# Optimization experiments

Hardware: AMD Instinct MI355X
Metric: run time of the kernel (lower is better)

The kernel has to match this reference:

```python
import jax, jax.numpy as jnp
import numpy as np

N_NODES = 50000
N_EDGES = 640000
N_GRAPHS = 64
IN_DIM, HID, OUT_DIM = 128, 256, 4


def gcn_conv(x, src, dst, W, b, n_nodes):
    """PyG GCNConv: linear transform, then sym-normalized aggregation with self-loops."""
    h = x @ W  # [N, out]
    deg = jnp.zeros((n_nodes,), h.dtype).at[dst].add(1.0) + 1.0  # +1 self-loop
    dinv = jax.lax.rsqrt(deg)  # deg >= 1 always
    norm = dinv[src] * dinv[dst]  # [E]
    msg = h[src] * norm[:, None]  # [E, out]  gather + scale
    agg = jax.ops.segment_sum(msg, dst, num_segments=n_nodes)  # scatter-add
    agg = agg + h * (dinv * dinv)[:, None]  # self-loop contribution
    return agg + b


def global_mean_pool(x, batch, num_graphs):
    s = jax.ops.segment_sum(x, batch, num_segments=num_graphs)
    cnt = jax.ops.segment_sum(jnp.ones((x.shape[0],), x.dtype), batch, num_segments=num_graphs)
    return s / jnp.clip(cnt, 1.0)[:, None]


def setup_inputs() -> dict:
    key = jax.random.key(0)
    ks = jax.random.split(key, 8)
    x = jax.random.normal(ks[0], (N_NODES, IN_DIM), jnp.float32)
    src = jax.random.randint(ks[1], (N_EDGES,), 0, N_NODES, jnp.int64 if jax.config.jax_enable_x64 else jnp.int32)
    dst = jax.random.randint(ks[2], (N_EDGES,), 0, N_NODES, src.dtype)
    batch = jnp.sort(jax.random.randint(ks[3], (N_NODES,), 0, N_GRAPHS, src.dtype))
    W1 = jax.random.normal(ks[4], (IN_DIM, HID), jnp.float32) * (1.0 / np.sqrt(IN_DIM))
    b1 = jnp.zeros((HID,), jnp.float32)
    W2 = jax.random.normal(ks[5], (HID, HID // 2), jnp.float32) * (1.0 / np.sqrt(HID))
    b2 = jnp.zeros((HID // 2,), jnp.float32)
    Wfc = jax.random.normal(ks[6], (HID // 2, OUT_DIM), jnp.float32) * (1.0 / np.sqrt(HID // 2))
    bfc = jnp.zeros((OUT_DIM,), jnp.float32)
    return {"x": x, "src": src, "dst": dst, "batch": batch,
            "W1": W1, "b1": b1, "W2": W2, "b2": b2, "Wfc": Wfc, "bfc": bfc}


def reference(x, src, dst, batch, W1, b1, W2, b2, Wfc, bfc):
    n = x.shape[0]
    h = jax.nn.relu(gcn_conv(x, src, dst, W1, b1, n))   # dropout is identity at inference
    h = jax.nn.relu(gcn_conv(h, src, dst, W2, b2, n))
    g = global_mean_pool(h, batch, N_GRAPHS)            # [G, HID//2]
    return g @ Wfc + bfc                                # [G, OUT_DIM]
```

## Files before the change

### kernel.cpp

```cpp
#include <hip/hip_runtime.h>


constexpr int IN_DIM  = 128;
constexpr int HID     = 256;
constexpr int HID2    = 128;
constexpr int OUT_DIM = 4;
constexpr int NGRAPH  = 64;
constexpr int TP      = 132;

typedef __attribute__((ext_vector_type(8))) short bf16x8;
typedef __attribute__((ext_vector_type(4))) float f32x4;

__device__ __forceinline__ short f2bf(float f) {
    union { float f; unsigned u; } v; v.f = f;
    unsigned r = v.u + 0x7fff + ((v.u >> 16) & 1);
    return (short)(r >> 16);
}
__device__ __forceinline__ float bf2f(short s) {
    union { unsigned u; float f; } v; v.u = ((unsigned)(unsigned short)s) << 16;
    return v.f;
}


__global__ void wprep_all_kernel(const float* __restrict__ W1, short* __restrict__ W1th,
                                 short* __restrict__ W1tl,
                                 const float* __restrict__ W2, short* __restrict__ W2th,
                                 short* __restrict__ W2tl,
                                 int* __restrict__ count, float* __restrict__ pool, int N) {
    int i = blockIdx.x * blockDim.x + threadIdx.x;
    if (i < IN_DIM * HID) {
        int k = i / HID, n = i % HID;
        float w = W1[i];
        short h = f2bf(w);
        W1th[n * IN_DIM + k] = h;
        W1tl[n * IN_DIM + k] = f2bf(w - bf2f(h));
    }
    if (i < HID * HID2) {
        int k = i / HID2, n = i % HID2;
        float w = W2[i];
        short h = f2bf(w);
        W2th[n * HID + k] = h;
        W2tl[n * HID + k] = f2bf(w - bf2f(h));
    }
    if (i < N) count[i] = 0;
    if (i < NGRAPH * HID2) pool[i] = 0.f;
}


__global__ void hist_kernel(const int* __restrict__ dst, int* __restrict__ count,
                            ushort* __restrict__ rank, int E) {
    int i = blockIdx.x * blockDim.x + threadIdx.x;
    if (i < E) rank[i] = (ushort)atomicAdd(&count[dst[i]], 1);
}

__global__ void scan1_kernel(const int* __restrict__ count, int* __restrict__ bsums, int N) {
    __shared__ int s[256];
    int t = threadIdx.x, i = blockIdx.x * 256 + t;
    int v = (i < N) ? count[i] : 0;
    s[t] = v; __syncthreads();
    for (int o = 1; o < 256; o <<= 1) {
        int x = (t >= o) ? s[t - o] : 0;
        __syncthreads(); s[t] += x; __syncthreads();
    }
    if (t == 255) bsums[blockIdx.x] = s[255];
}

__global__ void scan3_kernel(const int* __restrict__ count, const int* __restrict__ bsums,
                             int* __restrict__ rowptr, float* __restrict__ dinv,
                             int N, int E, int nb) {
    __shared__ int sb[256];
    __shared__ int s[256];
    int t = threadIdx.x, i = blockIdx.x * 256 + t;
    int bv = (t < nb) ? bsums[t] : 0;
    sb[t] = bv; __syncthreads();
    for (int o = 1; o < 256; o <<= 1) {
        int x = (t >= o) ? sb[t - o] : 0;
        __syncthreads(); sb[t] += x; __syncthreads();
    }
    int myex = (blockIdx.x == 0) ? 0 : sb[blockIdx.x - 1];
    int v = (i < N) ? count[i] : 0;
    s[t] = v; __syncthreads();
    for (int o = 1; o < 256; o <<= 1) {
        int x = (t >= o) ? s[t - o] : 0;
        __syncthreads(); s[t] += x; __syncthreads();
    }
    if (i < N) {
        rowptr[i] = myex + s[t] - v;
        dinv[i] = rsqrtf((float)v + 1.0f);
        if (i == 0) rowptr[N] = E;
    }
}

__global__ void scatter_scale_kernel(const int* __restrict__ src, const int* __restrict__ dst,
                                     const ushort* __restrict__ rank,
                                     const int* __restrict__ rowptr, ushort* __restrict__ csr,
                                     const float* __restrict__ x, const float* __restrict__ dinv,
                                     ushort* __restrict__ xb, int E, int total2) {
    int i = blockIdx.x * blockDim.x + threadIdx.x;
    if (i < E) {
        int p = rowptr[dst[i]] + (int)rank[i];
        csr[p] = (ushort)src[i];
    }
    if (i < total2) {
        float d = dinv[i >> 6];
        float2 v = ((const float2*)x)[i];
        ushort2 o;
        o.x = (ushort)f2bf(v.x * d);
        o.y = (ushort)f2bf(v.y * d);
        ((ushort2*)xb)[i] = o;
    }
}


template <int K, int N, bool ALO, bool RELU, bool SCALED>
__launch_bounds__(256)
__global__ void gemm_tile_kernel(const short* __restrict__ Ah, const short* __restrict__ Al,
                                 const short* __restrict__ Bh, const short* __restrict__ Bl,
                                 const float* __restrict__ bias,
                                 const float* __restrict__ dinv,
                                 short* __restrict__ Cb, int M) {
    __shared__ __align__(16) short LDSBUF[128 * TP];
    short (*S)[8][512] = (short (*)[8][512])LDSBUF;

    const int tid  = threadIdx.x;
    const int wave = tid >> 6;
    const int lane = tid & 63;
    const int row0 = blockIdx.y * 128;
    const int col0 = blockIdx.x * 128;

    const int l15 = lane & 15;
    const int kq  = (lane >> 4) * 8;

    f32x4 acc[4][4];
#pragma unroll
    for (int i = 0; i < 4; ++i)
#pragma unroll
        for (int j = 0; j < 4; ++j) acc[i][j] = f32x4{0.f, 0.f, 0.f, 0.f};

    const int mt0 = (wave & 1) * 4;
    const int nt0 = (wave >> 1) * 4;

    for (int kb = 0; kb < K; kb += 32) {
        if (ALO) {
            const short* gsrc = (wave == 0) ? Ah : (wave == 1) ? Al : (wave == 2) ? Bh : Bl;
            const bool isA = wave < 2;
            const int rb = (isA ? row0 : col0) + l15;
            bf16x8 stg[8];
#pragma unroll
            for (int j = 0; j < 8; ++j) {
                int rr = rb + j * 16;
                if (isA && rr >= M) rr = M - 1;
                stg[j] = *(const bf16x8*)(gsrc + (size_t)rr * K + kb + kq);
            }
#pragma unroll
            for (int j = 0; j < 8; ++j)
                *(bf16x8*)&S[wave][j][lane * 8] = stg[j];
        } else {
            if (wave < 2) {
                const int rb = row0 + l15;
                bf16x8 stg[4];
#pragma unroll
                for (int j = 0; j < 4; ++j) {
                    int rr = rb + (wave * 4 + j) * 16;
                    if (rr >= M) rr = M - 1;
                    stg[j] = *(const bf16x8*)(Ah + (size_t)rr * K + kb + kq);
                }
#pragma unroll
                for (int j = 0; j < 4; ++j)
                    *(bf16x8*)&S[0][wave * 4 + j][lane * 8] = stg[j];
            } else {
                const short* gsrc = (wave == 2) ? Bh : Bl;
                const int rb = col0 + l15;
                bf16x8 stg[8];
#pragma unroll
                for (int j = 0; j < 8; ++j)
                    stg[j] = *(const bf16x8*)(gsrc + (size_t)(rb + j * 16) * K + kb + kq);
#pragma unroll
                for (int j = 0; j < 8; ++j)
                    *(bf16x8*)&S[wave][j][lane * 8] = stg[j];
            }
        }
        __syncthreads();

        bf16x8 ah[4], al[4], bh[4], bl[4];
#pragma unroll
        for (int i = 0; i < 4; ++i) {
            ah[i] = *(const bf16x8*)&S[0][mt0 + i][lane * 8];
            if (ALO) al[i] = *(const bf16x8*)&S[1][mt0 + i][lane * 8];
            bh[i] = *(const bf16x8*)&S[2][nt0 + i][lane * 8];
            bl[i] = *(const bf16x8*)&S[3][nt0 + i][lane * 8];
        }
#pragma unroll
        for (int i = 0; i < 4; ++i)
#pragma unroll
            for (int j = 0; j < 4; ++j) {
                acc[i][j] = __builtin_amdgcn_mfma_f32_16x16x32_bf16(ah[i], bh[j], acc[i][j], 0, 0, 0);
                acc[i][j] = __builtin_amdgcn_mfma_f32_16x16x32_bf16(ah[i], bl[j], acc[i][j], 0, 0, 0);
                if (ALO)
                    acc[i][j] = __builtin_amdgcn_mfma_f32_16x16x32_bf16(al[i], bh[j], acc[i][j], 0, 0, 0);
            }
        __syncthreads();
    }

    short* T = LDSBUF;
    const int lrow_b = (wave & 1) * 64 + (lane >> 4) * 4;
    const int lcol_b = (wave >> 1) * 64 + l15;
#pragma unroll
    for (int j = 0; j < 4; ++j) {
        int lcol = lcol_b + j * 16;
        float bv = RELU ? bias[col0 + lcol] : 0.f;
#pragma unroll
        for (int i = 0; i < 4; ++i) {
#pragma unroll
            for (int r = 0; r < 4; ++r) {
                int lrow = lrow_b + i * 16 + r;
                float v = acc[i][j][r];
                if (RELU) v = fmaxf(v + bv, 0.f);
                if (SCALED) {
                    int dr = row0 + lrow; if (dr >= M) dr = M - 1;
                    v *= dinv[dr];
                }
                T[lrow * TP + lcol] = f2bf(v);
            }
        }
    }
    __syncthreads();
#pragma unroll
    for (int it = 0; it < 8; ++it) {
        int chunk = it * 256 + tid;
        int lr = chunk >> 4;
        int lc = (chunk & 15) * 8;
        int grow = row0 + lr;
        if (grow < M)
            *(bf16x8*)(Cb + (size_t)grow * N + col0 + lc) = *(const bf16x8*)&T[lr * TP + lc];
    }
}


template <bool POOL>
__launch_bounds__(256)
__global__ void agg_group_kernel(const ushort* __restrict__ hb, const float* __restrict__ dinv,
                                 const int* __restrict__ rowptr, const ushort* __restrict__ csr,
                                 const float* __restrict__ bias,
                                 short* __restrict__ oh,
                                 const int* __restrict__ batch, float* __restrict__ pool,
                                 int N) {
    __shared__ float pacc[16][128];
    __shared__ int   sgid[16];

    const int tid  = threadIdx.x;
    const int li   = tid & 15;
    const int nib  = tid >> 4;
    const int node = blockIdx.x * 16 + nib;
    const bool valid = node < N;
    const int cw = valid ? node : N - 1;

    const int lo = rowptr[cw], hi = rowptr[cw + 1];
    const float dd = dinv[cw];

    float a[8];
    {
        bf16x8 sv = *(const bf16x8*)(hb + ((size_t)cw << 7) + (li << 3));
#pragma unroll
        for (int d = 0; d < 8; ++d) a[d] = bf2f(sv[d]);
    }

    const ushort* hsl = hb + (li << 3);

    for (int base = lo; base < hi; base += 16) {
        int cnt = min(16, hi - base);
        int sidx = (int)csr[base + (li < cnt ? li : cnt - 1)];
        bf16x8 p[8], q[8];
#pragma unroll
        for (int u = 0; u < 8; ++u) {
            int s = __shfl(sidx, u < cnt ? u : cnt - 1, 16);
            p[u] = *(const bf16x8*)(hsl + ((size_t)s << 7));
        }
#pragma unroll
        for (int u = 0; u < 8; ++u) {
            int e = 8 + u;
            int s = __shfl(sidx, e < cnt ? e : cnt - 1, 16);
            q[u] = *(const bf16x8*)(hsl + ((size_t)s << 7));
        }
#pragma unroll
        for (int u = 0; u < 8; ++u) {
            bool v = u < cnt;
#pragma unroll
            for (int d = 0; d < 8; ++d) a[d] += v ? bf2f(p[u][d]) : 0.f;
        }
#pragma unroll
        for (int u = 0; u < 8; ++u) {
            bool v = 8 + u < cnt;
#pragma unroll
            for (int d = 0; d < 8; ++d) a[d] += v ? bf2f(q[u][d]) : 0.f;
        }
    }

#pragma unroll
    for (int d = 0; d < 8; ++d) a[d] *= dd;

    if (!POOL) {
        if (valid) {
            bf16x8 o;
#pragma unroll
            for (int d = 0; d < 8; ++d) o[d] = f2bf(a[d]);
            *(bf16x8*)&oh[(size_t)node * 128 + li * 8] = o;
        }
        return;
    }

    {
        float4 b0 = ((const float4*)bias)[li * 2];
        float4 b1 = ((const float4*)bias)[li * 2 + 1];
        a[0] = fmaxf(a[0] + b0.x, 0.f); a[1] = fmaxf(a[1] + b0.y, 0.f);
        a[2] = fmaxf(a[2] + b0.z, 0.f); a[3] = fmaxf(a[3] + b0.w, 0.f);
        a[4] = fmaxf(a[4] + b1.x, 0.f); a[5] = fmaxf(a[5] + b1.y, 0.f);
        a[6] = fmaxf(a[6] + b1.z, 0.f); a[7] = fmaxf(a[7] + b1.w, 0.f);
    }
    if (li == 0) sgid[nib] = valid ? batch[node] : -1;
#pragma unroll
    for (int d = 0; d < 8; ++d) pacc[nib][li * 8 + d] = a[d];
    __syncthreads();
    if (tid < 128) {
        int c = tid;
        int cur = sgid[0];
        float run = 0.f;
#pragma unroll 1
        for (int w = 0; w < 16; ++w) {
            int gi = sgid[w];
            if (gi < 0) break;
            if (gi != cur) { atomicAdd(&pool[cur * HID2 + c], run); run = 0.f; cur = gi; }
            run += pacc[w][c];
        }
        atomicAdd(&pool[cur * HID2 + c], run);
    }
}


__device__ __forceinline__ int lower_bound_i(const int* __restrict__ a, int n, int key) {
    int lo = 0, hi = n;
    while (lo < hi) {
        int mid = (lo + hi) >> 1;
        if (a[mid] < key) lo = mid + 1; else hi = mid;
    }
    return lo;
}

__global__ void fc_kernel(const float* __restrict__ pool, const int* __restrict__ batch,
                          const float* __restrict__ Wfc, const float* __restrict__ bfc,
                          float* __restrict__ out, int N) {
    int t = threadIdx.x;
    int g = t >> 2, o = t & 3;
    int lo = lower_bound_i(batch, N, g);
    int hi = lower_bound_i(batch, N, g + 1);
    float acc = 0.f;
#pragma unroll 8
    for (int c = 0; c < HID2; ++c)
        acc = fmaf(pool[g * HID2 + c], Wfc[c * OUT_DIM + o], acc);
    float inv = 1.0f / fmaxf((float)(hi - lo), 1.0f);
    out[g * OUT_DIM + o] = acc * inv + bfc[o];
}

extern "C" void kernel_launch(void* const* d_in, const int* in_sizes, int n_in,
                              void* d_out, int out_size, void* d_ws, size_t ws_size,
                              hipStream_t stream) {
    const float* x   = (const float*)d_in[0];
    const int* src   = (const int*)d_in[1];
    const int* dst   = (const int*)d_in[2];
    const int* batch = (const int*)d_in[3];
    const float* W1  = (const float*)d_in[4];
    const float* b1  = (const float*)d_in[5];
    const float* W2  = (const float*)d_in[6];
    const float* b2  = (const float*)d_in[7];
    const float* Wfc = (const float*)d_in[8];
    const float* bfc = (const float*)d_in[9];
    float* out = (float*)d_out;

    const int N = in_sizes[0] / IN_DIM;
    const int E = in_sizes[1];
    const int NB = (N + 255) / 256;
    const int GA = (N + 15) / 16;

    char* ws = (char*)d_ws;
    size_t off = 0;
    auto alloc = [&](size_t bytes) {
        char* p = ws + off;
        off = (off + bytes + 255) & ~(size_t)255;
        return p;
    };
    float*  dinv   = (float*) alloc((size_t)N * 4);
    int*    count  = (int*)   alloc((size_t)N * 4);
    int*    rowptr = (int*)   alloc((size_t)(N + 1) * 4);
    int*    bsums  = (int*)   alloc(256 * 4);
    ushort* rank   = (ushort*)alloc((size_t)E * 2);
    ushort* csr    = (ushort*)alloc((size_t)E * 2);
    short*  W1th   = (short*) alloc((size_t)IN_DIM * HID * 2);
    short*  W1tl   = (short*) alloc((size_t)IN_DIM * HID * 2);
    short*  W2th   = (short*) alloc((size_t)HID * HID2 * 2);
    short*  W2tl   = (short*) alloc((size_t)HID * HID2 * 2);
    ushort* xb     = (ushort*)alloc((size_t)N * IN_DIM * 2);
    short*  axb    = (short*) alloc((size_t)N * IN_DIM * 2);
    short*  a1h    = (short*) alloc((size_t)N * HID * 2);
    float*  pool   = (float*) alloc((size_t)NGRAPH * HID2 * 4);
    ushort* h2b = xb;

    wprep_all_kernel<<<(max(IN_DIM * HID, N) + 255) / 256, 256, 0, stream>>>(
        W1, W1th, W1tl, W2, W2th, W2tl, count, pool, N);

    hist_kernel<<<(E + 255) / 256, 256, 0, stream>>>(dst, count, rank, E);
    scan1_kernel<<<NB, 256, 0, stream>>>(count, bsums, N);
    scan3_kernel<<<NB, 256, 0, stream>>>(count, bsums, rowptr, dinv, N, E, NB);
    scatter_scale_kernel<<<(N * 64 + 255) / 256, 256, 0, stream>>>(
        src, dst, rank, rowptr, csr, x, dinv, xb, E, N * 64);

    agg_group_kernel<false><<<GA, 256, 0, stream>>>(
        xb, dinv, rowptr, csr, nullptr, axb, nullptr, nullptr, N);
    gemm_tile_kernel<IN_DIM, HID, false, true, false>
        <<<dim3(HID / 128, (N + 127) / 128), 256, 0, stream>>>(
        axb, nullptr, W1th, W1tl, b1, nullptr, a1h, N);

    gemm_tile_kernel<HID, HID2, false, false, true>
        <<<dim3(HID2 / 128, (N + 127) / 128), 256, 0, stream>>>(
        a1h, nullptr, W2th, W2tl, nullptr, dinv, (short*)h2b, N);
    agg_group_kernel<true><<<GA, 256, 0, stream>>>(
        h2b, dinv, rowptr, csr, b2, nullptr, batch, pool, N);

    fc_kernel<<<1, NGRAPH * OUT_DIM, 0, stream>>>(pool, batch, Wfc, bfc, out, N);
}
```

Baseline: 242.7 us.

## Fuse both dense GEMMs into one kernel keeping hidden activations in LDS

Replaces the two tiled GEMM launches with one fused kernel. Each block takes 64 rows, computes relu(A·W1+b1) into LDS, then multiplies by W2 and scales by dinv before writing bf16 output. This removes the N×256 bf16 intermediate round trip through global memory and one launch. In exchange, weight fragments are now read directly from global/L2 without LDS sharing, and there are fewer blocks (64-row tiles). The non-pooling aggregation kernel also returns early for out-of-range threads.

```diff
diff --git a/kernel.cpp b/kernel.cpp
--- a/kernel.cpp
+++ b/kernel.cpp
@@ -6,7 +6,6 @@
 constexpr int HID2    = 128;
 constexpr int OUT_DIM = 4;
 constexpr int NGRAPH  = 64;
-constexpr int TP      = 132;
 
 typedef __attribute__((ext_vector_type(8))) short bf16x8;
 typedef __attribute__((ext_vector_type(4))) float f32x4;
@@ -112,127 +111,130 @@
 }
 
 
-template <int K, int N, bool ALO, bool RELU, bool SCALED>
 __launch_bounds__(256)
-__global__ void gemm_tile_kernel(const short* __restrict__ Ah, const short* __restrict__ Al,
-                                 const short* __restrict__ Bh, const short* __restrict__ Bl,
-                                 const float* __restrict__ bias,
+__global__ void mlp_fused_kernel(const short* __restrict__ A,
+                                 const short* __restrict__ W1h, const short* __restrict__ W1l,
+                                 const float* __restrict__ b1,
+                                 const short* __restrict__ W2h, const short* __restrict__ W2l,
                                  const float* __restrict__ dinv,
                                  short* __restrict__ Cb, int M) {
-    __shared__ __align__(16) short LDSBUF[128 * TP];
-    short (*S)[8][512] = (short (*)[8][512])LDSBUF;
+    __shared__ __align__(16) short L[16384 + 8448];
+    short* A1 = L;
+    short* A0 = L + 16384;
+    __shared__ float dinv_s[64];
 
     const int tid  = threadIdx.x;
-    const int wave = tid >> 6;
+    const int w    = tid >> 6;
     const int lane = tid & 63;
-    const int row0 = blockIdx.y * 128;
-    const int col0 = blockIdx.x * 128;
-
-    const int l15 = lane & 15;
-    const int kq  = (lane >> 4) * 8;
-
-    f32x4 acc[4][4];
-#pragma unroll
-    for (int i = 0; i < 4; ++i)
-#pragma unroll
-        for (int j = 0; j < 4; ++j) acc[i][j] = f32x4{0.f, 0.f, 0.f, 0.f};
-
-    const int mt0 = (wave & 1) * 4;
-    const int nt0 = (wave >> 1) * 4;
-
-    for (int kb = 0; kb < K; kb += 32) {
-        if (ALO) {
-            const short* gsrc = (wave == 0) ? Ah : (wave == 1) ? Al : (wave == 2) ? Bh : Bl;
-            const bool isA = wave < 2;
-            const int rb = (isA ? row0 : col0) + l15;
-            bf16x8 stg[8];
-#pragma unroll
-            for (int j = 0; j < 8; ++j) {
-                int rr = rb + j * 16;
-                if (isA && rr >= M) rr = M - 1;
-                stg[j] = *(const bf16x8*)(gsrc + (size_t)rr * K + kb + kq);
+    const int l15  = lane & 15;
+    const int kq8  = (lane >> 4) * 8;
+    const int row0 = blockIdx.x * 64;
+
+    {
+        int rr = row0 + w * 16 + l15; if (rr >= M) rr = M - 1;
+        const short* ap = A + (size_t)rr * IN_DIM + kq8;
+        bf16x8 stg[4];
+#pragma unroll
+        for (int ks = 0; ks < 4; ++ks) stg[ks] = *(const bf16x8*)(ap + ks * 32);
+#pragma unroll
+        for (int ks = 0; ks < 4; ++ks) *(bf16x8*)&A0[(w * 4 + ks) * 512 + lane * 8] = stg[ks];
+    }
+    if (tid < 64) { int r = row0 + tid; dinv_s[tid] = dinv[r < M ? r : M - 1]; }
+    __syncthreads();
+
+    f32x4 acc1[4][4];
+#pragma unroll
+    for (int m = 0; m < 4; ++m)
+#pragma unroll
+        for (int n = 0; n < 4; ++n) acc1[m][n] = f32x4{0.f, 0.f, 0.f, 0.f};
+
+    const short* w1hp = W1h + (size_t)(w * 64 + l15) * IN_DIM + kq8;
+    const short* w1lp = W1l + (size_t)(w * 64 + l15) * IN_DIM + kq8;
+#pragma unroll
+    for (int ks = 0; ks < 4; ++ks) {
+        bf16x8 af[4], bh[4], bl[4];
+#pragma unroll
+        for (int m = 0; m < 4; ++m) af[m] = *(const bf16x8*)&A0[(m * 4 + ks) * 512 + lane * 8];
+#pragma unroll
+        for (int n = 0; n < 4; ++n) {
+            bh[n] = *(const bf16x8*)(w1hp + (size_t)(n * 16) * IN_DIM + ks * 32);
+            bl[n] = *(const bf16x8*)(w1lp + (size_t)(n * 16) * IN_DIM + ks * 32);
+        }
+#pragma unroll
+        for (int m = 0; m < 4; ++m)
+#pragma unroll
+            for (int n = 0; n < 4; ++n) {
+                acc1[m][n] = __builtin_amdgcn_mfma_f32_16x16x32_bf16(af[m], bh[n], acc1[m][n], 0, 0, 0);
+                acc1[m][n] = __builtin_amdgcn_mfma_f32_16x16x32_bf16(af[m], bl[n], acc1[m][n], 0, 0, 0);
             }
-#pragma unroll
-            for (int j = 0; j < 8; ++j)
-                *(bf16x8*)&S[wave][j][lane * 8] = stg[j];
-        } else {
-            if (wave < 2) {
-                const int rb = row0 + l15;
-                bf16x8 stg[4];
-#pragma unroll
-                for (int j = 0; j < 4; ++j) {
-                    int rr = rb + (wave * 4 + j) * 16;
-                    if (rr >= M) rr = M - 1;
-                    stg[j] = *(const bf16x8*)(Ah + (size_t)rr * K + kb + kq);
-                }
-#pragma unroll
-                for (int j = 0; j < 4; ++j)
-                    *(bf16x8*)&S[0][wave * 4 + j][lane * 8] = stg[j];
-            } else {
-                const short* gsrc = (wave == 2) ? Bh : Bl;
-                const int rb = col0 + l15;
-                bf16x8 stg[8];
-#pragma unroll
-                for (int j = 0; j < 8; ++j)
-                    stg[j] = *(const bf16x8*)(gsrc + (size_t)(rb + j * 16) * K + kb + kq);
-#pragma unroll
-                for (int j = 0; j < 8; ++j)
-                    *(bf16x8*)&S[wave][j][lane * 8] = stg[j];
+    }
+
+#pragma unroll
+    for (int n = 0; n < 4; ++n) {
+        int c  = w * 64 + n * 16 + l15;
+        float bv = b1[c];
+        int ks = c >> 5;
+        int q  = (c >> 3) & 3;
+        int e  = c & 7;
+#pragma unroll
+        for (int m = 0; m < 4; ++m)
+#pragma unroll
+            for (int r4 = 0; r4 < 4; ++r4) {
+                int rl = (lane >> 4) * 4 + r4;
+                float v = fmaxf(acc1[m][n][r4] + bv, 0.f);
+                A1[(m * 8 + ks) * 512 + (rl + 16 * q) * 8 + e] = f2bf(v);
             }
-        }
-        __syncthreads();
-
-        bf16x8 ah[4], al[4], bh[4], bl[4];
-#pragma unroll
-        for (int i = 0; i < 4; ++i) {
-            ah[i] = *(const bf16x8*)&S[0][mt0 + i][lane * 8];
-            if (ALO) al[i] = *(const bf16x8*)&S[1][mt0 + i][lane * 8];
-            bh[i] = *(const bf16x8*)&S[2][nt0 + i][lane * 8];
-            bl[i] = *(const bf16x8*)&S[3][nt0 + i][lane * 8];
-        }
-#pragma unroll
-        for (int i = 0; i < 4; ++i)
-#pragma unroll
-            for (int j = 0; j < 4; ++j) {
-                acc[i][j] = __builtin_amdgcn_mfma_f32_16x16x32_bf16(ah[i], bh[j], acc[i][j], 0, 0, 0);
-                acc[i][j] = __builtin_amdgcn_mfma_f32_16x16x32_bf16(ah[i], bl[j], acc[i][j], 0, 0, 0);
-                if (ALO)
-                    acc[i][j] = __builtin_amdgcn_mfma_f32_16x16x32_bf16(al[i], bh[j], acc[i][j], 0, 0, 0);
+    }
+    __syncthreads();
+
+    f32x4 acc2[4][2];
+#pragma unroll
+    for (int m = 0; m < 4; ++m)
+#pragma unroll
+        for (int n = 0; n < 2; ++n) acc2[m][n] = f32x4{0.f, 0.f, 0.f, 0.f};
+
+    const short* w2hp = W2h + (size_t)(w * 32 + l15) * HID + kq8;
+    const short* w2lp = W2l + (size_t)(w * 32 + l15) * HID + kq8;
+#pragma unroll
+    for (int ks = 0; ks < 8; ++ks) {
+        bf16x8 af[4], bh[2], bl[2];
+#pragma unroll
+        for (int m = 0; m < 4; ++m) af[m] = *(const bf16x8*)&A1[(m * 8 + ks) * 512 + lane * 8];
+#pragma unroll
+        for (int n = 0; n < 2; ++n) {
+            bh[n] = *(const bf16x8*)(w2hp + (size_t)(n * 16) * HID + ks * 32);
+            bl[n] = *(const bf16x8*)(w2lp + (size_t)(n * 16) * HID + ks * 32);
+        }
+#pragma unroll
+        for (int m = 0; m < 4; ++m)
+#pragma unroll
+            for (int n = 0; n < 2; ++n) {
+                acc2[m][n] = __builtin_amdgcn_mfma_f32_16x16x32_bf16(af[m], bh[n], acc2[m][n], 0, 0, 0);
+                acc2[m][n] = __builtin_amdgcn_mfma_f32_16x16x32_bf16(af[m], bl[n], acc2[m][n], 0, 0, 0);
             }
-        __syncthreads();
-    }
-
-    short* T = LDSBUF;
-    const int lrow_b = (wave & 1) * 64 + (lane >> 4) * 4;
-    const int lcol_b = (wave >> 1) * 64 + l15;
-#pragma unroll
-    for (int j = 0; j < 4; ++j) {
-        int lcol = lcol_b + j * 16;
-        float bv = RELU ? bias[col0 + lcol] : 0.f;
-#pragma unroll
-        for (int i = 0; i < 4; ++i) {
-#pragma unroll
-            for (int r = 0; r < 4; ++r) {
-                int lrow = lrow_b + i * 16 + r;
-                float v = acc[i][j][r];
-                if (RELU) v = fmaxf(v + bv, 0.f);
-                if (SCALED) {
-                    int dr = row0 + lrow; if (dr >= M) dr = M - 1;
-                    v *= dinv[dr];
-                }
-                T[lrow * TP + lcol] = f2bf(v);
+    }
+
+    short* T = A0;
+#pragma unroll
+    for (int n = 0; n < 2; ++n) {
+        int c = w * 32 + n * 16 + l15;
+#pragma unroll
+        for (int m = 0; m < 4; ++m)
+#pragma unroll
+            for (int r4 = 0; r4 < 4; ++r4) {
+                int r = m * 16 + (lane >> 4) * 4 + r4;
+                T[r * 132 + c] = f2bf(acc2[m][n][r4] * dinv_s[r]);
             }
-        }
     }
     __syncthreads();
 #pragma unroll
-    for (int it = 0; it < 8; ++it) {
+    for (int it = 0; it < 4; ++it) {
         int chunk = it * 256 + tid;
         int lr = chunk >> 4;
         int lc = (chunk & 15) * 8;
-        int grow = row0 + lr;
-        if (grow < M)
-            *(bf16x8*)(Cb + (size_t)grow * N + col0 + lc) = *(const bf16x8*)&T[lr * TP + lc];
+        int gr = row0 + lr;
+        if (gr < M)
+            *(bf16x8*)(Cb + (size_t)gr * HID2 + lc) = *(const bf16x8*)&T[lr * 132 + lc];
     }
 }
 
@@ -253,6 +255,7 @@
     const int nib  = tid >> 4;
     const int node = blockIdx.x * 16 + nib;
     const bool valid = node < N;
+    if (!POOL && !valid) return;
     const int cw = valid ? node : N - 1;
 
     const int lo = rowptr[cw], hi = rowptr[cw + 1];
@@ -380,6 +383,7 @@
     const int E = in_sizes[1];
     const int NB = (N + 255) / 256;
     const int GA = (N + 15) / 16;
+    const int GM = (N + 63) / 64;
 
     char* ws = (char*)d_ws;
     size_t off = 0;
@@ -400,7 +404,6 @@
     short*  W2tl   = (short*) alloc((size_t)HID * HID2 * 2);
     ushort* xb     = (ushort*)alloc((size_t)N * IN_DIM * 2);
     short*  axb    = (short*) alloc((size_t)N * IN_DIM * 2);
-    short*  a1h    = (short*) alloc((size_t)N * HID * 2);
     float*  pool   = (float*) alloc((size_t)NGRAPH * HID2 * 4);
     ushort* h2b = xb;
 
@@ -415,13 +418,10 @@
 
     agg_group_kernel<false><<<GA, 256, 0, stream>>>(
         xb, dinv, rowptr, csr, nullptr, axb, nullptr, nullptr, N);
-    gemm_tile_kernel<IN_DIM, HID, false, true, false>
-        <<<dim3(HID / 128, (N + 127) / 128), 256, 0, stream>>>(
-        axb, nullptr, W1th, W1tl, b1, nullptr, a1h, N);
-
-    gemm_tile_kernel<HID, HID2, false, false, true>
-        <<<dim3(HID2 / 128, (N + 127) / 128), 256, 0, stream>>>(
-        a1h, nullptr, W2th, W2tl, nullptr, dinv, (short*)h2b, N);
+
+    mlp_fused_kernel<<<GM, 256, 0, stream>>>(
+        axb, W1th, W1tl, b1, W2th, W2tl, dinv, (short*)h2b, N);
+
     agg_group_kernel<true><<<GA, 256, 0, stream>>>(
         h2b, dinv, rowptr, csr, b2, nullptr, batch, pool, N);
 
```

Result: no change. 240.0 us (-1.1%).
